# Kernel optimization log

Hardware: AMD Instinct MI355X
Metric: run time of the kernel (lower is better)

The kernel has to match this reference:

```python
import jax, jax.numpy as jnp
import numpy as np

B, S, HID = 2, 2048, 2048
NH, G = 32, 4            # num_attn_heads, num_attn_groups
HD = HID // NH           # 64 head_dim
HKV = NH // G            # 8 query/key heads
THETA = 10000.0


def setup_inputs() -> dict:
    key = jax.random.key(0)
    k1, k2, k3, k4 = jax.random.split(key, 4)
    s = 0.02
    return {
        "hidden_states": jax.random.normal(k1, (B, S, HID), jnp.float32),
        "position_ids": jnp.broadcast_to(jnp.arange(S, dtype=jnp.int32)[None, :], (B, S)),
        "Wq": jax.random.normal(k2, (HID, HKV * HD), jnp.float32) * s,
        "Wk": jax.random.normal(k3, (HID, HKV * HD), jnp.float32) * s,
        "Wv": jax.random.normal(k4, (HID, NH * HD), jnp.float32) * s,
    }


def _rotate_half(x):
    x1, x2 = jnp.split(x, 2, axis=-1)
    return jnp.concatenate([-x2, x1], axis=-1)


def reference(hidden_states, position_ids, Wq, Wk, Wv):
    b, s, hid = hidden_states.shape
    # Q/K use HKV heads, V uses all NH heads
    Q = (hidden_states @ Wq).reshape(b, s, HKV, HD)
    K = (hidden_states @ Wk).reshape(b, s, HKV, HD)
    V = (hidden_states @ Wv).reshape(b, s, NH, HD)

    # RoPE (seq_len <= max_position_embeddings, no NTK rescale branch)
    inv_freq = 1.0 / (THETA ** (jnp.arange(0, HD, 2, dtype=jnp.float32) / HD))
    freqs = position_ids.astype(jnp.float32)[:, :, None] * inv_freq[None, None, :]  # [B,S,HD/2]
    emb = jnp.concatenate([freqs, freqs], axis=-1)                                   # [B,S,HD]
    cos = jnp.cos(emb)[:, :, None, :]  # unsqueeze head dim
    sin = jnp.sin(emb)[:, :, None, :]
    Q = Q * cos + _rotate_half(Q) * sin
    K = K * cos + _rotate_half(K) * sin

    # repeat_qk: [B,S,HKV,HD] -> [B,S,G*HKV,HD], head index = r*HKV + h
    def rep(x):
        return jnp.broadcast_to(x[:, :, None, :, :], (b, s, G, HKV, HD)).reshape(b, s, NH, HD)
    Q = rep(Q)
    K = rep(K)

    # causal SDPA
    scale = 1.0 / np.sqrt(HD).astype(np.float32)
    scores = jnp.einsum('bqhd,bkhd->bhqk', Q, K) * scale          # [B,NH,S,S]
    causal = jnp.tril(jnp.ones((s, s), dtype=bool))
    scores = jnp.where(causal[None, None, :, :], scores, jnp.float32(-1e9))
    attn = jax.nn.softmax(scores, axis=-1)
    out = jnp.einsum('bhqk,bkhd->bqhd', attn, V)                  # [B,S,NH,HD]
    return out.reshape(b, s, hid)
```

## Files before the change

### kernel.cpp

```cpp
#include <hip/hip_runtime.h>
#include <hip/hip_bf16.h>

typedef unsigned short u16;
typedef unsigned int   u32;
typedef __attribute__((ext_vector_type(8))) short bf16x8;
typedef __attribute__((ext_vector_type(4))) float f32x4;

#define B_   2
#define S_   2048
#define HID_ 2048
#define NH_  32
#define HKV_ 8
#define HD_  64
#define NQK  512
#define NTOT 3072
#define MROWS 4096

__device__ __forceinline__ u16 f2bf(float f) {
  u32 x = __float_as_uint(f);
  x += 0x7fffu + ((x >> 16) & 1u);
  return (u16)(x >> 16);
}
__device__ __forceinline__ float bf2f(u16 u) { return __uint_as_float(((u32)u) << 16); }
__device__ __forceinline__ u32 pack2bf(float a, float b) {
  return (u32)f2bf(a) | ((u32)f2bf(b) << 16);
}

__device__ __forceinline__ void gload16(const u16* g, u16* l) {
  __builtin_amdgcn_global_load_lds((const __attribute__((address_space(1))) void*)g,
                                   (__attribute__((address_space(3))) void*)l, 16, 0, 0);
}

__global__ __launch_bounds__(256) void cvtA_kernel(const float* __restrict__ A,
                                                   u16* __restrict__ Abf) {
  const int n4 = (MROWS * HID_) / 4;
  int i = blockIdx.x * blockDim.x + threadIdx.x;
  for (int idx = i; idx < n4; idx += gridDim.x * blockDim.x) {
    float4 v = ((const float4*)A)[idx];
    ushort4 o;
    o.x = f2bf(v.x); o.y = f2bf(v.y); o.z = f2bf(v.z); o.w = f2bf(v.w);
    ((ushort4*)Abf)[idx] = o;
  }
}

__global__ __launch_bounds__(256) void cvtW_kernel(const float* __restrict__ Wq,
                                                   const float* __restrict__ Wk,
                                                   const float* __restrict__ Wv,
                                                   u16* __restrict__ Wt) {
  int n0 = blockIdx.x * 32, k0 = blockIdx.y * 32;
  const float* src; int ld, nn;
  if (n0 < 512)       { src = Wq; nn = n0;        ld = 512;  }
  else if (n0 < 1024) { src = Wk; nn = n0 - 512;  ld = 512;  }
  else                { src = Wv; nn = n0 - 1024; ld = 2048; }
  __shared__ float tile[32][33];
  int tx = threadIdx.x, ty = threadIdx.y;
#pragma unroll
  for (int i = 0; i < 4; i++) {
    int kk = k0 + ty + i * 8;
    tile[ty + i * 8][tx] = src[(size_t)kk * ld + nn + tx];
  }
  __syncthreads();
#pragma unroll
  for (int i = 0; i < 4; i++) {
    int nrow = ty + i * 8;
    Wt[(size_t)(n0 + nrow) * HID_ + k0 + tx] = f2bf(tile[tx][nrow]);
  }
}

__global__ __launch_bounds__(256) void gemm_kernel(const u16* __restrict__ A,
                                                   const u16* __restrict__ Bt,
                                                   u16* __restrict__ C) {
  __shared__ u16 As[128 * 64];
  __shared__ u16 Bs[128 * 64];
  bf16x8* Asv = (bf16x8*)As;
  bf16x8* Bsv = (bf16x8*)Bs;
  int tid = threadIdx.x, l = tid & 63, wid = tid >> 6;
  int l15 = l & 15, lg = l >> 4;
  int bm = blockIdx.y * 128, bn = blockIdx.x * 128;
  int wr = (wid >> 1) * 64, wc = (wid & 1) * 64;
  f32x4 acc[4][4] = {};
  int r_[4], c_[4];
#pragma unroll
  for (int i = 0; i < 4; i++) {
    int slot = i * 256 + tid;
    int r = slot >> 3, sub = slot & 7;
    r_[i] = r;
    c_[i] = (sub ^ (r & 7)) << 3;
  }
  for (int kt = 0; kt < HID_ / 64; kt++) {
    int k0 = kt * 64;
    __syncthreads();
#pragma unroll
    for (int i = 0; i < 4; i++)
      gload16(A + (size_t)(bm + r_[i]) * HID_ + k0 + c_[i], (u16*)&Asv[i * 256 + wid * 64]);
#pragma unroll
    for (int i = 0; i < 4; i++)
      gload16(Bt + (size_t)(bn + r_[i]) * HID_ + k0 + c_[i], (u16*)&Bsv[i * 256 + wid * 64]);
    __syncthreads();
#pragma unroll
    for (int kc = 0; kc < 2; kc++) {
      bf16x8 af[4], bfr[4];
      int sub = kc * 4 + lg;
#pragma unroll
      for (int m = 0; m < 4; m++) {
        int row = wr + m * 16 + l15;
        af[m] = Asv[row * 8 + (sub ^ (row & 7))];
      }
#pragma unroll
      for (int n = 0; n < 4; n++) {
        int row = wc + n * 16 + l15;
        bfr[n] = Bsv[row * 8 + (sub ^ (row & 7))];
      }
#pragma unroll
      for (int m = 0; m < 4; m++)
#pragma unroll
        for (int n = 0; n < 4; n++)
          acc[m][n] = __builtin_amdgcn_mfma_f32_16x16x32_bf16(af[m], bfr[n], acc[m][n], 0, 0, 0);
    }
  }
#pragma unroll
  for (int m = 0; m < 4; m++)
#pragma unroll
    for (int n = 0; n < 4; n++) {
      int col  = bn + wc + n * 16 + l15;
      int rowb = bm + wr + m * 16 + lg * 4;
#pragma unroll
      for (int j = 0; j < 4; j++)
        C[(size_t)(rowb + j) * NTOT + col] = f2bf(acc[m][n][j]);
    }
}

__global__ __launch_bounds__(128) void rope_kernel(const u16* __restrict__ QKV,
                                                   const int* __restrict__ pos_ids,
                                                   u16* __restrict__ Qr,
                                                   u16* __restrict__ Kr) {
  int bs = blockIdx.x;
  int b = bs >> 11, s = bs & 2047;
  __shared__ float cs[32], sn[32];
  int t = threadIdx.x;
  if (t < 32) {
    float inv = expf(-((float)(2 * t) / 64.0f) * logf(10000.0f));
    float ang = (float)pos_ids[bs] * inv;
    cs[t] = cosf(ang);
    sn[t] = sinf(ang);
  }
  __syncthreads();
  const u16* row = QKV + (size_t)bs * NTOT;
#pragma unroll
  for (int i = 0; i < 4; i++) {
    int e = t + i * 128;
    int h = e >> 6, d = e & 63, j = d & 31;
    int ep = (d < 32) ? e + 32 : e - 32;
    size_t dst = (((size_t)(b * HKV_ + h) * S_ + s) * HD_) + d;
    float xq = bf2f(row[e]),        xq2 = bf2f(row[ep]);
    float xk = bf2f(row[NQK + e]),  xk2 = bf2f(row[NQK + ep]);
    float qv = (d < 32) ? xq * cs[j] - xq2 * sn[j] : xq * cs[j] + xq2 * sn[j];
    float kv = (d < 32) ? xk * cs[j] - xk2 * sn[j] : xk * cs[j] + xk2 * sn[j];
    Qr[dst] = f2bf(qv * 0.125f);
    Kr[dst] = f2bf(kv);
  }
}

__global__ __launch_bounds__(256) void transV_kernel(const u16* __restrict__ QKV,
                                                     u16* __restrict__ Vt) {
  int st = blockIdx.x, h = blockIdx.y, b = blockIdx.z;
  __shared__ u16 tile[64][65];
  int t = threadIdx.x;
#pragma unroll
  for (int i = 0; i < 16; i++) {
    int idx = t + i * 256;
    int r = idx >> 6, d = idx & 63;
    tile[r][d] = QKV[(size_t)(b * S_ + st * 64 + r) * NTOT + 1024 + h * 64 + d];
  }
  __syncthreads();
#pragma unroll
  for (int i = 0; i < 16; i++) {
    int idx = t + i * 256;
    int d = idx >> 6, ss = idx & 63;
    Vt[((size_t)(b * NH_ + h) * HD_ + d) * S_ + st * 64 + ss] = tile[ss][d];
  }
}

__global__ __launch_bounds__(64, 1) void attn_kernel(const u16* __restrict__ Qr,
                                                     const u16* __restrict__ Kr,
                                                     const u16* __restrict__ Vt,
                                                     float* __restrict__ Out) {
  int bx = blockIdx.x;
  int hk = blockIdx.y, b = blockIdx.z;
  int qt = ((hk >> 2) & 1) ? (63 - bx) : bx;
  int l = threadIdx.x, l15 = l & 15, g = l >> 4;
  int qb = qt * 32;

  __shared__ u16 Plds[32 * 64];

  const u16* Qbase = Qr + (size_t)(b * HKV_ + hk) * S_ * HD_;
  const u16* Kbase = Kr + (size_t)(b * HKV_ + hk) * S_ * HD_;
  const u16* Vb[4];
#pragma unroll
  for (int r = 0; r < 4; r++)
    Vb[r] = Vt + (size_t)(b * NH_ + r * 8 + hk) * HD_ * S_;

  bf16x8 bq[2][2];
#pragma unroll
  for (int nq = 0; nq < 2; nq++)
#pragma unroll
    for (int kc = 0; kc < 2; kc++)
      bq[nq][kc] = *(const bf16x8*)(Qbase + (size_t)(qb + nq * 16 + l15) * HD_ + kc * 32 + g * 8);

  f32x4 O[4][2][4] = {};
  float mS[2] = {-1e30f, -1e30f}, lS[2] = {0.f, 0.f};

  int ntiles = (qb + 95) >> 6;

  bf16x8 ka[2][4];
#pragma unroll
  for (int kc = 0; kc < 2; kc++)
#pragma unroll
    for (int mk = 0; mk < 4; mk++)
      ka[kc][mk] = *(const bf16x8*)(Kbase + (size_t)(mk * 16 + l15) * HD_ + kc * 32 + g * 8);

  for (int kt = 0; kt < ntiles; kt++) {
    f32x4 sacc[4][2] = {};
#pragma unroll
    for (int kc = 0; kc < 2; kc++)
#pragma unroll
      for (int mk = 0; mk < 4; mk++)
#pragma unroll
        for (int nq = 0; nq < 2; nq++)
          sacc[mk][nq] = __builtin_amdgcn_mfma_f32_16x16x32_bf16(ka[kc][mk], bq[nq][kc], sacc[mk][nq], 0, 0, 0);
    int ktn = (kt + 1 < ntiles) ? kt + 1 : kt;
    bf16x8 kan[2][4];
#pragma unroll
    for (int kc = 0; kc < 2; kc++)
#pragma unroll
      for (int mk = 0; mk < 4; mk++)
        kan[kc][mk] = *(const bf16x8*)(Kbase + (size_t)(ktn * 64 + mk * 16 + l15) * HD_ + kc * 32 + g * 8);
    float tmax[2] = {-1e30f, -1e30f};
#pragma unroll
    for (int mk = 0; mk < 4; mk++)
#pragma unroll
      for (int nq = 0; nq < 2; nq++)
#pragma unroll
        for (int j = 0; j < 4; j++) {
          int key = kt * 64 + mk * 16 + g * 4 + j;
          int q   = qb + nq * 16 + l15;
          float s = (key <= q) ? sacc[mk][nq][j] : -1e30f;
          sacc[mk][nq][j] = s;
          tmax[nq] = fmaxf(tmax[nq], s);
        }
#pragma unroll
    for (int nq = 0; nq < 2; nq++) {
      tmax[nq] = fmaxf(tmax[nq], __shfl_xor(tmax[nq], 16));
      tmax[nq] = fmaxf(tmax[nq], __shfl_xor(tmax[nq], 32));
    }
    bool need = (tmax[0] > mS[0] + 8.0f) || (tmax[1] > mS[1] + 8.0f);
    if (__any(need)) {
      float alpha[2];
#pragma unroll
      for (int nq = 0; nq < 2; nq++) {
        float mnew = fmaxf(mS[nq], tmax[nq]);
        alpha[nq] = __expf(mS[nq] - mnew);
        mS[nq] = mnew;
        lS[nq] *= alpha[nq];
      }
#pragma unroll
      for (int m = 0; m < 2; m++)
#pragma unroll
        for (int j = 0; j < 4; j++) {
          float a = __shfl(alpha[m], g * 4 + j);
#pragma unroll
          for (int r = 0; r < 4; r++)
#pragma unroll
            for (int nd = 0; nd < 4; nd++)
              O[r][m][nd][j] *= a;
        }
    }
    float tsum[2] = {0.f, 0.f};
    u32 upk[2][4][2];
#pragma unroll
    for (int nq = 0; nq < 2; nq++)
#pragma unroll
      for (int mk = 0; mk < 4; mk++) {
        float p0 = __expf(sacc[mk][nq][0] - mS[nq]);
        float p1 = __expf(sacc[mk][nq][1] - mS[nq]);
        float p2 = __expf(sacc[mk][nq][2] - mS[nq]);
        float p3 = __expf(sacc[mk][nq][3] - mS[nq]);
        tsum[nq] += (p0 + p1) + (p2 + p3);
        upk[nq][mk][0] = pack2bf(p0, p1);
        upk[nq][mk][1] = pack2bf(p2, p3);
      }
#pragma unroll
    for (int nq = 0; nq < 2; nq++) {
      tsum[nq] += __shfl_xor(tsum[nq], 16);
      tsum[nq] += __shfl_xor(tsum[nq], 32);
      lS[nq] += tsum[nq];
    }
#pragma unroll
    for (int nq = 0; nq < 2; nq++)
#pragma unroll
      for (int mk = 0; mk < 4; mk++) {
        int ql  = nq * 16 + l15;
        int sub = mk * 2 + (g >> 1);
        int byteoff = ql * 128 + ((sub ^ (ql & 7)) * 16) + (g & 1) * 8;
        *(uint2*)((char*)Plds + byteoff) = make_uint2(upk[nq][mk][0], upk[nq][mk][1]);
      }
#pragma unroll
    for (int kc = 0; kc < 2; kc++) {
      bf16x8 pa[2];
#pragma unroll
      for (int m = 0; m < 2; m++) {
        int ql  = m * 16 + l15;
        int sub = kc * 4 + g;
        pa[m] = *(bf16x8*)((char*)Plds + ql * 128 + ((sub ^ (ql & 7)) * 16));
      }
#pragma unroll
      for (int r = 0; r < 4; r++) {
        bf16x8 vb[4];
#pragma unroll
        for (int nd = 0; nd < 4; nd++) {
          int d = nd * 16 + l15;
          vb[nd] = *(const bf16x8*)(Vb[r] + (size_t)d * S_ + kt * 64 + kc * 32 + g * 8);
        }
#pragma unroll
        for (int m = 0; m < 2; m++)
#pragma unroll
          for (int nd = 0; nd < 4; nd++)
            O[r][m][nd] = __builtin_amdgcn_mfma_f32_16x16x32_bf16(pa[m], vb[nd], O[r][m][nd], 0, 0, 0);
      }
    }
#pragma unroll
    for (int kc = 0; kc < 2; kc++)
#pragma unroll
      for (int mk = 0; mk < 4; mk++)
        ka[kc][mk] = kan[kc][mk];
  }
  float linv[2];
#pragma unroll
  for (int m = 0; m < 2; m++) linv[m] = 1.0f / lS[m];
#pragma unroll
  for (int m = 0; m < 2; m++)
#pragma unroll
    for (int j = 0; j < 4; j++) {
      float li = __shfl(linv[m], g * 4 + j);
      int q = qb + m * 16 + g * 4 + j;
#pragma unroll
      for (int r = 0; r < 4; r++)
#pragma unroll
        for (int nd = 0; nd < 4; nd++) {
          int d = nd * 16 + l15;
          Out[(size_t)(b * S_ + q) * HID_ + (r * 8 + hk) * 64 + d] = O[r][m][nd][j] * li;
        }
    }
}

extern "C" void kernel_launch(void* const* d_in, const int* in_sizes, int n_in,
                              void* d_out, int out_size, void* d_ws, size_t ws_size,
                              hipStream_t stream) {
  const float* hs  = (const float*)d_in[0];
  const int*   pos = (const int*)d_in[1];
  const float* Wq  = (const float*)d_in[2];
  const float* Wk  = (const float*)d_in[3];
  const float* Wv  = (const float*)d_in[4];
  float* out = (float*)d_out;
  char* ws = (char*)d_ws;
  u16* Abf = (u16*)(ws + 0);
  u16* Wt  = (u16*)(ws + 16777216);
  u16* QKV = (u16*)(ws + 29360128);
  u16* Qr  = (u16*)(ws + 54525952);
  u16* Kr  = (u16*)(ws + 58720256);
  u16* Vt  = (u16*)(ws + 62914560);

  cvtA_kernel<<<dim3(2048), dim3(256), 0, stream>>>(hs, Abf);
  cvtW_kernel<<<dim3(96, 64), dim3(32, 8), 0, stream>>>(Wq, Wk, Wv, Wt);
  gemm_kernel<<<dim3(24, 32), dim3(256), 0, stream>>>(Abf, Wt, QKV);
  rope_kernel<<<dim3(4096), dim3(128), 0, stream>>>(QKV, pos, Qr, Kr);
  transV_kernel<<<dim3(32, 32, 2), dim3(256), 0, stream>>>(QKV, Vt);
  attn_kernel<<<dim3(64, 8, 2), dim3(64), 0, stream>>>(Qr, Kr, Vt, out);
}
```

Before: 286.5 us.

## Pipeline QK scores ahead in attention, vectorize RoPE, remap GEMM and attention grids

The attention loop now computes the next tile's QK^T scores while the current tile's softmax and PV run, prefetches K two tiles ahead, and raises wave priority around the MFMA blocks. The attention grid is flattened so the heaviest causal query tiles are scheduled first. The GEMM grid is remapped so consecutive blocks map to XCD-friendly tile groups, and the RoPE kernel now uses 16-byte vector loads and stores. Together these aim to hide latency and improve scheduling, at the cost of extra registers from double-buffered score accumulators.

```diff
diff --git a/kernel.cpp b/kernel.cpp
--- a/kernel.cpp
+++ b/kernel.cpp
@@ -76,7 +76,9 @@
   bf16x8* Bsv = (bf16x8*)Bs;
   int tid = threadIdx.x, l = tid & 63, wid = tid >> 6;
   int l15 = l & 15, lg = l >> 4;
-  int bm = blockIdx.y * 128, bn = blockIdx.x * 128;
+  int orig = (blockIdx.x & 7) * 96 + (blockIdx.x >> 3);
+  int bxx = orig % 24, byy = orig / 24;
+  int bm = byy * 128, bn = bxx * 128;
   int wr = (wid >> 1) * 64, wc = (wid & 1) * 64;
   f32x4 acc[4][4] = {};
   int r_[4], c_[4];
@@ -146,19 +148,23 @@
   }
   __syncthreads();
   const u16* row = QKV + (size_t)bs * NTOT;
-#pragma unroll
-  for (int i = 0; i < 4; i++) {
-    int e = t + i * 128;
-    int h = e >> 6, d = e & 63, j = d & 31;
-    int ep = (d < 32) ? e + 32 : e - 32;
-    size_t dst = (((size_t)(b * HKV_ + h) * S_ + s) * HD_) + d;
-    float xq = bf2f(row[e]),        xq2 = bf2f(row[ep]);
-    float xk = bf2f(row[NQK + e]),  xk2 = bf2f(row[NQK + ep]);
-    float qv = (d < 32) ? xq * cs[j] - xq2 * sn[j] : xq * cs[j] + xq2 * sn[j];
-    float kv = (d < 32) ? xk * cs[j] - xk2 * sn[j] : xk * cs[j] + xk2 * sn[j];
-    Qr[dst] = f2bf(qv * 0.125f);
-    Kr[dst] = f2bf(kv);
-  }
+  int part = t >> 6;
+  int g2 = t & 63;
+  int h = g2 >> 3, seg = (g2 >> 2) & 1, d0 = (g2 & 3) * 8;
+  const u16* src = row + part * NQK + h * 64;
+  bf16x8 v = *(const bf16x8*)(src + seg * 32 + d0);
+  bf16x8 p = *(const bf16x8*)(src + (1 - seg) * 32 + d0);
+  float scale = part ? 1.0f : 0.125f;
+  u16 ov[8];
+#pragma unroll
+  for (int i = 0; i < 8; i++) {
+    int j = d0 + i;
+    float a = bf2f((u16)v[i]), q = bf2f((u16)p[i]);
+    float r = seg ? (a * cs[j] + q * sn[j]) : (a * cs[j] - q * sn[j]);
+    ov[i] = f2bf(r * scale);
+  }
+  u16* dst = (part ? Kr : Qr) + (((size_t)(b * HKV_ + h) * S_ + s) * HD_) + seg * 32 + d0;
+  *(bf16x8*)dst = *(bf16x8*)ov;
 }
 
 __global__ __launch_bounds__(256) void transV_kernel(const u16* __restrict__ QKV,
@@ -185,9 +191,10 @@
                                                      const u16* __restrict__ Kr,
                                                      const u16* __restrict__ Vt,
                                                      float* __restrict__ Out) {
-  int bx = blockIdx.x;
-  int hk = blockIdx.y, b = blockIdx.z;
-  int qt = ((hk >> 2) & 1) ? (63 - bx) : bx;
+  int bid = blockIdx.x;
+  int c  = bid & 15;
+  int hk = c & 7, b = c >> 3;
+  int qt = 63 - (bid >> 4);
   int l = threadIdx.x, l15 = l & 15, g = l >> 4;
   int qb = qt * 32;
 
@@ -218,23 +225,41 @@
 #pragma unroll
     for (int mk = 0; mk < 4; mk++)
       ka[kc][mk] = *(const bf16x8*)(Kbase + (size_t)(mk * 16 + l15) * HD_ + kc * 32 + g * 8);
+  f32x4 scur[4][2] = {};
+#pragma unroll
+  for (int kc = 0; kc < 2; kc++)
+#pragma unroll
+    for (int mk = 0; mk < 4; mk++)
+#pragma unroll
+      for (int nq = 0; nq < 2; nq++)
+        scur[mk][nq] = __builtin_amdgcn_mfma_f32_16x16x32_bf16(ka[kc][mk], bq[nq][kc], scur[mk][nq], 0, 0, 0);
+  int t1 = (ntiles > 1) ? 1 : 0;
+#pragma unroll
+  for (int kc = 0; kc < 2; kc++)
+#pragma unroll
+    for (int mk = 0; mk < 4; mk++)
+      ka[kc][mk] = *(const bf16x8*)(Kbase + (size_t)(t1 * 64 + mk * 16 + l15) * HD_ + kc * 32 + g * 8);
 
   for (int kt = 0; kt < ntiles; kt++) {
-    f32x4 sacc[4][2] = {};
+    int tp = (kt + 2 < ntiles) ? kt + 2 : ntiles - 1;
+    bf16x8 kan[2][4];
 #pragma unroll
     for (int kc = 0; kc < 2; kc++)
 #pragma unroll
       for (int mk = 0; mk < 4; mk++)
-#pragma unroll
-        for (int nq = 0; nq < 2; nq++)
-          sacc[mk][nq] = __builtin_amdgcn_mfma_f32_16x16x32_bf16(ka[kc][mk], bq[nq][kc], sacc[mk][nq], 0, 0, 0);
-    int ktn = (kt + 1 < ntiles) ? kt + 1 : kt;
-    bf16x8 kan[2][4];
-#pragma unroll
-    for (int kc = 0; kc < 2; kc++)
-#pragma unroll
-      for (int mk = 0; mk < 4; mk++)
-        kan[kc][mk] = *(const bf16x8*)(Kbase + (size_t)(ktn * 64 + mk * 16 + l15) * HD_ + kc * 32 + g * 8);
+        kan[kc][mk] = *(const bf16x8*)(Kbase + (size_t)(tp * 64 + mk * 16 + l15) * HD_ + kc * 32 + g * 8);
+    f32x4 snxt[4][2] = {};
+    if (kt + 1 < ntiles) {
+      __builtin_amdgcn_s_setprio(1);
+#pragma unroll
+      for (int kc = 0; kc < 2; kc++)
+#pragma unroll
+        for (int mk = 0; mk < 4; mk++)
+#pragma unroll
+          for (int nq = 0; nq < 2; nq++)
+            snxt[mk][nq] = __builtin_amdgcn_mfma_f32_16x16x32_bf16(ka[kc][mk], bq[nq][kc], snxt[mk][nq], 0, 0, 0);
+      __builtin_amdgcn_s_setprio(0);
+    }
     float tmax[2] = {-1e30f, -1e30f};
 #pragma unroll
     for (int mk = 0; mk < 4; mk++)
@@ -244,8 +269,8 @@
         for (int j = 0; j < 4; j++) {
           int key = kt * 64 + mk * 16 + g * 4 + j;
           int q   = qb + nq * 16 + l15;
-          float s = (key <= q) ? sacc[mk][nq][j] : -1e30f;
-          sacc[mk][nq][j] = s;
+          float s = (key <= q) ? scur[mk][nq][j] : -1e30f;
+          scur[mk][nq][j] = s;
           tmax[nq] = fmaxf(tmax[nq], s);
         }
 #pragma unroll
@@ -281,10 +306,10 @@
     for (int nq = 0; nq < 2; nq++)
 #pragma unroll
       for (int mk = 0; mk < 4; mk++) {
-        float p0 = __expf(sacc[mk][nq][0] - mS[nq]);
-        float p1 = __expf(sacc[mk][nq][1] - mS[nq]);
-        float p2 = __expf(sacc[mk][nq][2] - mS[nq]);
-        float p3 = __expf(sacc[mk][nq][3] - mS[nq]);
+        float p0 = __expf(scur[mk][nq][0] - mS[nq]);
+        float p1 = __expf(scur[mk][nq][1] - mS[nq]);
+        float p2 = __expf(scur[mk][nq][2] - mS[nq]);
+        float p3 = __expf(scur[mk][nq][3] - mS[nq]);
         tsum[nq] += (p0 + p1) + (p2 + p3);
         upk[nq][mk][0] = pack2bf(p0, p1);
         upk[nq][mk][1] = pack2bf(p2, p3);
@@ -304,6 +329,7 @@
         int byteoff = ql * 128 + ((sub ^ (ql & 7)) * 16) + (g & 1) * 8;
         *(uint2*)((char*)Plds + byteoff) = make_uint2(upk[nq][mk][0], upk[nq][mk][1]);
       }
+    __builtin_amdgcn_s_setprio(1);
 #pragma unroll
     for (int kc = 0; kc < 2; kc++) {
       bf16x8 pa[2];
@@ -328,11 +354,17 @@
             O[r][m][nd] = __builtin_amdgcn_mfma_f32_16x16x32_bf16(pa[m], vb[nd], O[r][m][nd], 0, 0, 0);
       }
     }
+    __builtin_amdgcn_s_setprio(0);
 #pragma unroll
     for (int kc = 0; kc < 2; kc++)
 #pragma unroll
       for (int mk = 0; mk < 4; mk++)
         ka[kc][mk] = kan[kc][mk];
+#pragma unroll
+    for (int mk = 0; mk < 4; mk++)
+#pragma unroll
+      for (int nq = 0; nq < 2; nq++)
+        scur[mk][nq] = snxt[mk][nq];
   }
   float linv[2];
 #pragma unroll
@@ -372,8 +404,8 @@
 
   cvtA_kernel<<<dim3(2048), dim3(256), 0, stream>>>(hs, Abf);
   cvtW_kernel<<<dim3(96, 64), dim3(32, 8), 0, stream>>>(Wq, Wk, Wv, Wt);
-  gemm_kernel<<<dim3(24, 32), dim3(256), 0, stream>>>(Abf, Wt, QKV);
+  gemm_kernel<<<dim3(768), dim3(256), 0, stream>>>(Abf, Wt, QKV);
   rope_kernel<<<dim3(4096), dim3(128), 0, stream>>>(QKV, pos, Qr, Kr);
   transV_kernel<<<dim3(32, 32, 2), dim3(256), 0, stream>>>(QKV, Vt);
-  attn_kernel<<<dim3(64, 8, 2), dim3(64), 0, stream>>>(Qr, Kr, Vt, out);
-}
+  attn_kernel<<<dim3(1024), dim3(64), 0, stream>>>(Qr, Kr, Vt, out);
+}
```

New measurement: 297.3 us. 3.8% more time.
